# Kernel optimization log

Measured on AMD Instinct MI355X. Metric: run time of the kernel, lower is better.

Reference implementation:

```python
import jax, jax.numpy as jnp
import numpy as np

NUM_USERS = 100000
NUM_ITEMS = 200000
EMB_DIM = 64
NUM_LAYERS = 3
NUM_INTER = 1000000
BATCH = 16384


def setup_inputs() -> dict:
    key = jax.random.key(0)
    k1, k2, k3, k4, k5, k6, k7 = jax.random.split(key, 7)
    # xavier-uniform-ish init for embeddings
    bound_u = float(np.sqrt(6.0 / (NUM_USERS + EMB_DIM)))
    bound_i = float(np.sqrt(6.0 / (NUM_ITEMS + EMB_DIM)))
    user_emb = jax.random.uniform(k1, (NUM_USERS, EMB_DIM), jnp.float32, -bound_u, bound_u)
    item_emb = jax.random.uniform(k2, (NUM_ITEMS, EMB_DIM), jnp.float32, -bound_i, bound_i)
    layer_weights = jax.random.uniform(k3, (NUM_LAYERS + 1,), jnp.float32)
    inter_users = jax.random.randint(k4, (NUM_INTER,), 0, NUM_USERS, jnp.int32)
    inter_items = jax.random.randint(k5, (NUM_INTER,), 0, NUM_ITEMS, jnp.int32)
    user_ids = jax.random.randint(k6, (BATCH,), 0, NUM_USERS, jnp.int32)
    item_ids = jax.random.randint(k7, (BATCH,), 0, NUM_ITEMS, jnp.int32)
    return {
        "user_emb": user_emb,
        "item_emb": item_emb,
        "layer_weights": layer_weights,
        "inter_users": inter_users,
        "inter_items": inter_items,
        "user_ids": user_ids,
        "item_ids": item_ids,
    }


def reference(user_emb, item_emb, layer_weights, inter_users, inter_items, user_ids, item_ids):
    n_users = user_emb.shape[0]
    n_items = item_emb.shape[0]
    n_nodes = n_users + n_items

    # Symmetrized bipartite edge list: (u -> i+n_users) and (i+n_users -> u)
    rows = inter_users
    cols = inter_items + n_users
    src = jnp.concatenate([rows, cols])  # [2E]
    dst = jnp.concatenate([cols, rows])  # [2E]

    # Symmetric degree normalization: D^{-1/2} A D^{-1/2}
    deg = jax.ops.segment_sum(jnp.ones_like(src, dtype=jnp.float32), src,
                              num_segments=n_nodes)
    dinv = jnp.where(deg > 0, jax.lax.rsqrt(jnp.maximum(deg, 1.0)) * (deg > 0), 0.0)
    dinv = jnp.where(deg > 0, deg ** -0.5, 0.0)
    edge_w = dinv[src] * dinv[dst]  # [2E]

    emb = jnp.concatenate([user_emb, item_emb], axis=0)  # [N, D]
    weights = jax.nn.softmax(layer_weights)

    final = weights[0] * emb
    for layer in range(NUM_LAYERS):
        # SpMM: out[src] += w * emb[dst]
        emb = jax.ops.segment_sum(edge_w[:, None] * emb[dst], src,
                                  num_segments=n_nodes)
        final = final + weights[layer + 1] * emb

    u_final = final[:n_users]
    i_final = final[n_users:]

    user_vectors = u_final[user_ids]   # [B, D]
    item_vectors = i_final[item_ids]   # [B, D]
    scores = jnp.sum(user_vectors * item_vectors, axis=1)  # [B]
    return scores
```

## Files before the change

kernel.cpp:

```cpp
#include <hip/hip_runtime.h>
#include <math.h>

#define NUM_USERS 100000
#define NUM_ITEMS 200000
#define N_NODES   300000
#define EMB       64
#define NUM_INTER 1000000
#define N_EDGES   (2 * NUM_INTER)
#define MAX_SLOTS (N_EDGES + 3 * N_NODES + 16)
#define BATCH     16384

#define BSHIFT 9
#define BNODES 512
#define NBKT   ((N_NODES + BNODES - 1) / BNODES)
#define CAP    6144
#define EDGES_PER_BLOCK 4096
#define AB_BLOCKS ((NUM_INTER + EDGES_PER_BLOCK - 1) / EDGES_PER_BLOCK)

#define CONV_BLOCKS ((N_NODES * 8 + 255) / 256)
#define MARK_BLOCKS ((BATCH * 2) / 256)
#define PROP_BLOCKS ((N_NODES * 8 + 255) / 256)

typedef float    vfloat4 __attribute__((ext_vector_type(4)));
typedef int      vint4   __attribute__((ext_vector_type(4)));
typedef _Float16 half8   __attribute__((ext_vector_type(8)));

__global__ __launch_bounds__(256) void bucket_scatter_k(
        const int* __restrict__ iu, const int* __restrict__ ii,
        int* __restrict__ cursor , uint2* __restrict__ pairs) {
    __shared__ int hist[NBKT];
    __shared__ int gbase[NBKT];
    int tid = threadIdx.x;
    for (int b = tid; b < NBKT; b += 256) hist[b] = 0;
    __syncthreads();

    int e0 = blockIdx.x * EDGES_PER_BLOCK;
    int u[16], it[16];
    unsigned pk[32];
    #pragma unroll
    for (int k = 0; k < 16; ++k) {
        int e = e0 + k * 256 + tid;
        bool v = (e < NUM_INTER);
        u[k]  = v ? iu[e] : -1;
        it[k] = v ? (NUM_USERS + ii[e]) : -1;
    }
    #pragma unroll
    for (int k = 0; k < 16; ++k) {
        if (u[k] >= 0) {
            int b0 = u[k] >> BSHIFT;
            int r0 = atomicAdd(&hist[b0], 1);
            pk[2 * k] = ((unsigned)b0 << 13) | (unsigned)r0;
            int b1 = it[k] >> BSHIFT;
            int r1 = atomicAdd(&hist[b1], 1);
            pk[2 * k + 1] = ((unsigned)b1 << 13) | (unsigned)r1;
        }
    }
    __syncthreads();
    for (int b = tid; b < NBKT; b += 256) {
        int c = hist[b];
        if (c) gbase[b] = atomicAdd(&cursor[b * 16], c);
    }
    __syncthreads();
    #pragma unroll
    for (int k = 0; k < 16; ++k) {
        if (u[k] >= 0) {
            unsigned p0 = pk[2 * k];
            int b0 = (int)(p0 >> 13);
            int s0 = gbase[b0] + (int)(p0 & 0x1fffu);
            if (s0 < CAP) pairs[(size_t)b0 * CAP + s0] = make_uint2((unsigned)u[k], (unsigned)it[k]);
            unsigned p1 = pk[2 * k + 1];
            int b1 = (int)(p1 >> 13);
            int s1 = gbase[b1] + (int)(p1 & 0x1fffu);
            if (s1 < CAP) pairs[(size_t)b1 * CAP + s1] = make_uint2((unsigned)it[k], (unsigned)u[k]);
        }
    }
}

__global__ __launch_bounds__(256) void bucket_deg_k(
        const int* __restrict__ cursor, const uint2* __restrict__ pairs,
        int* __restrict__ deg, float* __restrict__ dinv, float* __restrict__ d2,
        float* __restrict__ rcp, int* __restrict__ lofs, int* __restrict__ bkt_padded) {
    __shared__ int cnt[BNODES];
    __shared__ int sc[256];
    int b = blockIdx.x, tid = threadIdx.x;
    cnt[tid] = 0; cnt[tid + 256] = 0;
    __syncthreads();
    int n = cursor[b * 16]; if (n > CAP) n = CAP;
    const uint2* p = pairs + (size_t)b * CAP;
    for (int j = tid; j < n; j += 256)
        atomicAdd(&cnt[p[j].x & (BNODES - 1)], 1);
    __syncthreads();

    int l0 = 2 * tid, l1 = 2 * tid + 1;
    int c0 = cnt[l0], c1 = cnt[l1];
    int p0 = (c0 + 3) & ~3, p1 = (c1 + 3) & ~3;
    int s = p0 + p1;
    sc[tid] = s;
    __syncthreads();
    for (int o = 1; o < 256; o <<= 1) {
        int x = (tid >= o) ? sc[tid - o] : 0;
        __syncthreads();
        sc[tid] += x;
        __syncthreads();
    }
    int excl = sc[tid] - s;
    int g0 = (b << BSHIFT) + l0;
    int g1 = g0 + 1;
    if (g0 < N_NODES) {
        deg[g0] = c0;
        float fd = (float)c0;
        dinv[g0] = (c0 > 0) ? (1.0f / sqrtf(fd)) : 0.0f;
        d2[g0]   = (c0 > 0) ? (1.0f / fd) : 0.0f;
        rcp[g0]  = (c0 > 0) ? sqrtf(fd) : 0.0f;
        lofs[g0] = excl;
    }
    if (g1 < N_NODES) {
        deg[g1] = c1;
        float fd = (float)c1;
        dinv[g1] = (c1 > 0) ? (1.0f / sqrtf(fd)) : 0.0f;
        d2[g1]   = (c1 > 0) ? (1.0f / fd) : 0.0f;
        rcp[g1]  = (c1 > 0) ? sqrtf(fd) : 0.0f;
        lofs[g1] = excl + p0;
    }
    if (tid == 255) bkt_padded[b] = sc[255];
}

__global__ void csr_mid_k(const int* __restrict__ bkt_padded, int* __restrict__ bkt_base,
                          int* __restrict__ row_start,
                          const float* __restrict__ lw, float* __restrict__ w,
                          _Float16* __restrict__ semb, _Float16* __restrict__ z1,
                          _Float16* __restrict__ z2) {
    __shared__ int lds[1024];
    int t = threadIdx.x;
    int v = (t < NBKT) ? bkt_padded[t] : 0;
    lds[t] = v;
    __syncthreads();
    for (int o = 1; o < 1024; o <<= 1) {
        int x = (t >= o) ? lds[t - o] : 0;
        __syncthreads();
        lds[t] += x;
        __syncthreads();
    }
    if (t < NBKT) bkt_base[t] = lds[t] - v;
    if (t == 1023) row_start[N_NODES] = lds[1023];
    if (t < 96) {
        unsigned* p = (t < 32) ? (unsigned*)semb : (t < 64) ? (unsigned*)z1 : (unsigned*)z2;
        p[(size_t)N_NODES * 32 + (t & 31)] = 0u;
    }
    if (t == 0) {
        float a = lw[0], b = lw[1], c = lw[2], d = lw[3];
        float m = fmaxf(fmaxf(a, b), fmaxf(c, d));
        float e0 = expf(a - m), e1 = expf(b - m), e2 = expf(c - m), e3 = expf(d - m);
        float sm = e0 + e1 + e2 + e3;
        w[0] = e0 / sm; w[1] = e1 / sm; w[2] = e2 / sm; w[3] = e3 / sm;
    }
}

__global__ __launch_bounds__(256) void bucket_build_k(
        const int* __restrict__ cursor, const uint2* __restrict__ pairs,
        const int* __restrict__ bkt_base, const int* __restrict__ lofs,
        int* __restrict__ row_start, int* __restrict__ nbr,
        const float* __restrict__ dinv,
        const float* __restrict__ ue, const float* __restrict__ ie,
        _Float16* __restrict__ semb) {
    int bid = blockIdx.x;
    int tid = threadIdx.x;
    if (bid >= NBKT) {
        int t = (bid - NBKT) * 256 + tid;
        int node = t >> 3;
        int q = t & 7;
        if (node >= N_NODES) return;
        const float4* src = (node < NUM_USERS)
            ? (const float4*)ue + (size_t)node * 16
            : (const float4*)ie + (size_t)(node - NUM_USERS) * 16;
        float4 f0 = src[q * 2];
        float4 f1 = src[q * 2 + 1];
        float s = dinv[node];
        half8 h;
        h[0] = (_Float16)(s * f0.x); h[1] = (_Float16)(s * f0.y);
        h[2] = (_Float16)(s * f0.z); h[3] = (_Float16)(s * f0.w);
        h[4] = (_Float16)(s * f1.x); h[5] = (_Float16)(s * f1.y);
        h[6] = (_Float16)(s * f1.z); h[7] = (_Float16)(s * f1.w);
        ((half8*)semb)[(size_t)node * 8 + q] = h;
        return;
    }
    __shared__ int ofs[BNODES];
    __shared__ int cnt2[BNODES];
    int b = bid;
    int base = bkt_base[b];
    {
        int g0 = (b << BSHIFT) + tid;
        int g1 = g0 + 256;
        int o0 = (g0 < N_NODES) ? lofs[g0] : 0;
        int o1 = (g1 < N_NODES) ? lofs[g1] : 0;
        ofs[tid] = o0; ofs[tid + 256] = o1;
        cnt2[tid] = 0; cnt2[tid + 256] = 0;
        if (g0 < N_NODES) row_start[g0] = base + o0;
        if (g1 < N_NODES) row_start[g1] = base + o1;
    }
    __syncthreads();
    int n = cursor[b * 16]; if (n > CAP) n = CAP;
    const uint2* p = pairs + (size_t)b * CAP;
    for (int j = tid; j < n; j += 256) {
        uint2 pr = p[j];
        int l = (int)(pr.x & (BNODES - 1));
        int r = atomicAdd(&cnt2[l], 1);
        nbr[base + ofs[l] + r] = (int)pr.y;
    }
}

__global__ void mark_prop_k(const int* __restrict__ row_start, const int* __restrict__ nbr,
                            const int* __restrict__ deg, const float* __restrict__ d2,
                            const _Float16* __restrict__ semb, _Float16* __restrict__ z1,
                            const int* __restrict__ uid, const int* __restrict__ iid,
                            int* __restrict__ flag) {
    int bid = blockIdx.x;
    if (bid < MARK_BLOCKS) {
        int t = bid * 256 + threadIdx.x;
        int slot = t >> 1;
        int node = (t & 1) ? (NUM_USERS + iid[slot]) : uid[slot];
        flag[node] = 1;
        int beg = row_start[node];
        int lim = beg + deg[node];
        for (int j = beg; j < lim; ++j) flag[nbr[j]] = 1;
        return;
    }
    int t = (bid - MARK_BLOCKS) * 256 + threadIdx.x;
    int node = t >> 3;
    int q = t & 7;
    if (node >= N_NODES) return;
    int beg = row_start[node], end = row_start[node + 1];
    int lim = beg + deg[node];
    const half8* src = (const half8*)semb;
    float a0 = 0.f, a1 = 0.f, a2 = 0.f, a3 = 0.f, a4 = 0.f, a5 = 0.f, a6 = 0.f, a7 = 0.f;
    for (int j = beg; j < end; j += 8) {
        vint4 na = __builtin_nontemporal_load((const vint4*)(nbr + j));
        vint4 nb = __builtin_nontemporal_load((const vint4*)(nbr + j + 4));
        #pragma unroll
        for (int k = 0; k < 8; ++k) {
            int id = (j + k < lim) ? ((k < 4) ? na[k] : nb[k - 4]) : N_NODES;
            half8 h = src[(size_t)id * 8 + q];
            a0 += (float)h[0]; a1 += (float)h[1]; a2 += (float)h[2]; a3 += (float)h[3];
            a4 += (float)h[4]; a5 += (float)h[5]; a6 += (float)h[6]; a7 += (float)h[7];
        }
    }
    float s = d2[node];
    half8 r;
    r[0] = (_Float16)(s * a0); r[1] = (_Float16)(s * a1);
    r[2] = (_Float16)(s * a2); r[3] = (_Float16)(s * a3);
    r[4] = (_Float16)(s * a4); r[5] = (_Float16)(s * a5);
    r[6] = (_Float16)(s * a6); r[7] = (_Float16)(s * a7);
    __builtin_nontemporal_store(r, (half8*)z1 + (size_t)node * 8 + q);
}

__global__ void prop_masked_k(const int* __restrict__ row_start, const int* __restrict__ nbr,
                              const int* __restrict__ deg, const float* __restrict__ d2,
                              const int* __restrict__ flag,
                              const _Float16* __restrict__ in, _Float16* __restrict__ out) {
    int t = blockIdx.x * blockDim.x + threadIdx.x;
    int node = t >> 3;
    int q = t & 7;
    if (node >= N_NODES) return;
    if (!flag[node]) return;
    int beg = row_start[node], end = row_start[node + 1];
    int lim = beg + deg[node];
    const half8* src = (const half8*)in;
    float a0 = 0.f, a1 = 0.f, a2 = 0.f, a3 = 0.f, a4 = 0.f, a5 = 0.f, a6 = 0.f, a7 = 0.f;
    for (int j = beg; j < end; j += 8) {
        vint4 na = __builtin_nontemporal_load((const vint4*)(nbr + j));
        vint4 nb = __builtin_nontemporal_load((const vint4*)(nbr + j + 4));
        #pragma unroll
        for (int k = 0; k < 8; ++k) {
            int id = (j + k < lim) ? ((k < 4) ? na[k] : nb[k - 4]) : N_NODES;
            half8 h = src[(size_t)id * 8 + q];
            a0 += (float)h[0]; a1 += (float)h[1]; a2 += (float)h[2]; a3 += (float)h[3];
            a4 += (float)h[4]; a5 += (float)h[5]; a6 += (float)h[6]; a7 += (float)h[7];
        }
    }
    float s = d2[node];
    half8 r;
    r[0] = (_Float16)(s * a0); r[1] = (_Float16)(s * a1);
    r[2] = (_Float16)(s * a2); r[3] = (_Float16)(s * a3);
    r[4] = (_Float16)(s * a4); r[5] = (_Float16)(s * a5);
    r[6] = (_Float16)(s * a6); r[7] = (_Float16)(s * a7);
    __builtin_nontemporal_store(r, (half8*)out + (size_t)node * 8 + q);
}

__global__ void fused_score_k(const int* __restrict__ row_start, const int* __restrict__ nbr,
                              const int* __restrict__ deg,
                              const float* __restrict__ dinv, const float* __restrict__ rcp,
                              const float* __restrict__ ue, const float* __restrict__ ie,
                              const _Float16* __restrict__ z1, const _Float16* __restrict__ z2,
                              const int* __restrict__ uid, const int* __restrict__ iid,
                              const float* __restrict__ w4, float* __restrict__ out) {
    int t = blockIdx.x * blockDim.x + threadIdx.x;
    int slot = t >> 4;
    if (slot >= BATCH) return;
    int within = t & 15;
    int side = within >> 3;
    int q = within & 7;

    int node;
    const float4* erow;
    if (side == 0) {
        int u = uid[slot];
        node = u;
        erow = (const float4*)ue + (size_t)u * 16;
    } else {
        int ii_ = iid[slot];
        node = NUM_USERS + ii_;
        erow = (const float4*)ie + (size_t)ii_ * 16;
    }

    float w0 = w4[0], w1 = w4[1], w2 = w4[2], w3 = w4[3];
    int beg = row_start[node], end = row_start[node + 1];
    int lim = beg + deg[node];
    const half8* z2v = (const half8*)z2;

    float a0 = 0.f, a1 = 0.f, a2 = 0.f, a3 = 0.f, a4 = 0.f, a5 = 0.f, a6 = 0.f, a7 = 0.f;
    for (int j = beg; j < end; j += 8) {
        vint4 na = __builtin_nontemporal_load((const vint4*)(nbr + j));
        vint4 nb = __builtin_nontemporal_load((const vint4*)(nbr + j + 4));
        #pragma unroll
        for (int k = 0; k < 8; ++k) {
            int id = (j + k < lim) ? ((k < 4) ? na[k] : nb[k - 4]) : N_NODES;
            half8 h = z2v[(size_t)id * 8 + q];
            a0 += (float)h[0]; a1 += (float)h[1]; a2 += (float)h[2]; a3 += (float)h[3];
            a4 += (float)h[4]; a5 += (float)h[5]; a6 += (float)h[6]; a7 += (float)h[7];
        }
    }

    float r  = rcp[node];
    float di = dinv[node];
    float e[8];
    *reinterpret_cast<float4*>(&e[0]) = erow[q * 2];
    *reinterpret_cast<float4*>(&e[4]) = erow[q * 2 + 1];
    half8 h1 = ((const half8*)z1)[(size_t)node * 8 + q];
    half8 h2 = z2v[(size_t)node * 8 + q];
    float acc[8] = {a0, a1, a2, a3, a4, a5, a6, a7};

    float f[8];
    #pragma unroll
    for (int d = 0; d < 8; ++d)
        f[d] = w0 * e[d] + r * (w1 * (float)h1[d] + w2 * (float)h2[d]) + w3 * di * acc[d];

    float p = 0.f;
    #pragma unroll
    for (int d = 0; d < 8; ++d) {
        float o = __shfl_xor(f[d], 8);
        p += f[d] * o;
    }
    p += __shfl_xor(p, 1);
    p += __shfl_xor(p, 2);
    p += __shfl_xor(p, 4);

    if (within == 0) out[slot] = p;
}


extern "C" void kernel_launch(void* const* d_in, const int* in_sizes, int n_in,
                              void* d_out, int out_size, void* d_ws, size_t ws_size,
                              hipStream_t stream) {
    const float* user_emb = (const float*)d_in[0];
    const float* item_emb = (const float*)d_in[1];
    const float* layer_w  = (const float*)d_in[2];
    const int*   inter_u  = (const int*)d_in[3];
    const int*   inter_i  = (const int*)d_in[4];
    const int*   user_ids = (const int*)d_in[5];
    const int*   item_ids = (const int*)d_in[6];
    float* out = (float*)d_out;

    char* base = (char*)d_ws;
    size_t off = 0;
    auto alloc = [&](size_t bytes) -> char* {
        char* p = base + off;
        off = (off + bytes + 255) & ~(size_t)255;
        return p;
    };
    float*    w4        = (float*)    alloc(4 * sizeof(float));
    int*      deg       = (int*)      alloc((size_t)N_NODES * sizeof(int));
    float*    dinv      = (float*)    alloc((size_t)N_NODES * sizeof(float));
    float*    d2        = (float*)    alloc((size_t)N_NODES * sizeof(float));
    float*    rcp       = (float*)    alloc((size_t)N_NODES * sizeof(float));
    int*      lofs      = (int*)      alloc((size_t)N_NODES * sizeof(int));
    int*      row_start = (int*)      alloc(((size_t)N_NODES + 1) * sizeof(int));
    int*      bkt_pad   = (int*)      alloc((size_t)NBKT * sizeof(int));
    int*      bkt_base  = (int*)      alloc((size_t)NBKT * sizeof(int));
    int*      flag      = (int*)      alloc((size_t)N_NODES * sizeof(int));
    int*      cursor    = (int*)      alloc((size_t)NBKT * 16 * sizeof(int));
    uint2*    pairs     = (uint2*)    alloc((size_t)NBKT * CAP * sizeof(uint2));
    int*      csr_nbr   = (int*)      alloc((size_t)MAX_SLOTS * sizeof(int));
    _Float16* semb      = (_Float16*) alloc(((size_t)N_NODES + 1) * EMB * sizeof(_Float16));
    _Float16* zA        = (_Float16*) alloc(((size_t)N_NODES + 1) * EMB * sizeof(_Float16));
    _Float16* zB        = (_Float16*) alloc(((size_t)N_NODES + 1) * EMB * sizeof(_Float16));

    size_t span = (size_t)((char*)cursor - (char*)flag) + (size_t)NBKT * 16 * sizeof(int);
    hipMemsetAsync(flag, 0, span, stream);

    bucket_scatter_k<<<AB_BLOCKS, 256, 0, stream>>>(inter_u, inter_i, cursor, pairs);

    bucket_deg_k<<<NBKT, 256, 0, stream>>>(cursor, pairs, deg, dinv, d2, rcp, lofs, bkt_pad);

    csr_mid_k<<<1, 1024, 0, stream>>>(bkt_pad, bkt_base, row_start, layer_w, w4, semb, zB, zA);

    bucket_build_k<<<NBKT + CONV_BLOCKS, 256, 0, stream>>>(
        cursor, pairs, bkt_base, lofs, row_start, csr_nbr, dinv, user_emb, item_emb, semb);

    mark_prop_k<<<MARK_BLOCKS + PROP_BLOCKS, 256, 0, stream>>>(
        row_start, csr_nbr, deg, d2, semb, zB, user_ids, item_ids, flag);

    prop_masked_k<<<PROP_BLOCKS, 256, 0, stream>>>(
        row_start, csr_nbr, deg, d2, flag, zB, zA);

    fused_score_k<<<(BATCH * 16 + 255) / 256, 256, 0, stream>>>(
        row_start, csr_nbr, deg, dinv, rcp, user_emb, item_emb,
        zB , zA , user_ids, item_ids, w4, out);
}
```

Baseline: 280.4 us.

## Pack bucket pairs into 32-bit codes and move neighbor marking into bucket pass

```diff
diff --git a/kernel.cpp b/kernel.cpp
--- a/kernel.cpp
+++ b/kernel.cpp
@@ -6,8 +6,7 @@
 #define N_NODES   300000
 #define EMB       64
 #define NUM_INTER 1000000
-#define N_EDGES   (2 * NUM_INTER)
-#define MAX_SLOTS (N_EDGES + 3 * N_NODES + 16)
+#define MAX_SLOTS (2 * NUM_INTER + 3 * N_NODES + 16)
 #define BATCH     16384
 
 #define BSHIFT 9
@@ -16,25 +15,36 @@
 #define CAP    6144
 #define EDGES_PER_BLOCK 4096
 #define AB_BLOCKS ((NUM_INTER + EDGES_PER_BLOCK - 1) / EDGES_PER_BLOCK)
+#define QMARK_BLOCKS ((BATCH * 2) / 256)
 
 #define CONV_BLOCKS ((N_NODES * 8 + 255) / 256)
-#define MARK_BLOCKS ((BATCH * 2) / 256)
 #define PROP_BLOCKS ((N_NODES * 8 + 255) / 256)
 
-typedef float    vfloat4 __attribute__((ext_vector_type(4)));
-typedef int      vint4   __attribute__((ext_vector_type(4)));
-typedef _Float16 half8   __attribute__((ext_vector_type(8)));
+typedef int      vint4 __attribute__((ext_vector_type(4)));
+typedef _Float16 half8 __attribute__((ext_vector_type(8)));
+
+#define PMASK 0x7FFFFu
 
 __global__ __launch_bounds__(256) void bucket_scatter_k(
         const int* __restrict__ iu, const int* __restrict__ ii,
-        int* __restrict__ cursor , uint2* __restrict__ pairs) {
+        const int* __restrict__ uid, const int* __restrict__ iid,
+        int* __restrict__ cursor , unsigned* __restrict__ pairs,
+        unsigned char* __restrict__ qflag, int* __restrict__ flag) {
+    int tid = threadIdx.x;
+    if (blockIdx.x < QMARK_BLOCKS) {
+        int t = blockIdx.x * 256 + tid;
+        int node = (t & 1) ? (NUM_USERS + iid[t >> 1]) : uid[t >> 1];
+        qflag[node] = 1;
+        flag[node]  = 1;
+        return;
+    }
     __shared__ int hist[NBKT];
     __shared__ int gbase[NBKT];
-    int tid = threadIdx.x;
+    int bid = blockIdx.x - QMARK_BLOCKS;
     for (int b = tid; b < NBKT; b += 256) hist[b] = 0;
     __syncthreads();
 
-    int e0 = blockIdx.x * EDGES_PER_BLOCK;
+    int e0 = bid * EDGES_PER_BLOCK;
     int u[16], it[16];
     unsigned pk[32];
     #pragma unroll
@@ -67,28 +77,41 @@
             unsigned p0 = pk[2 * k];
             int b0 = (int)(p0 >> 13);
             int s0 = gbase[b0] + (int)(p0 & 0x1fffu);
-            if (s0 < CAP) pairs[(size_t)b0 * CAP + s0] = make_uint2((unsigned)u[k], (unsigned)it[k]);
+            if (s0 < CAP)
+                pairs[(size_t)b0 * CAP + s0] =
+                    ((unsigned)(u[k] & (BNODES - 1)) << 19) | (unsigned)it[k];
             unsigned p1 = pk[2 * k + 1];
             int b1 = (int)(p1 >> 13);
             int s1 = gbase[b1] + (int)(p1 & 0x1fffu);
-            if (s1 < CAP) pairs[(size_t)b1 * CAP + s1] = make_uint2((unsigned)it[k], (unsigned)u[k]);
+            if (s1 < CAP)
+                pairs[(size_t)b1 * CAP + s1] =
+                    ((unsigned)(it[k] & (BNODES - 1)) << 19) | (unsigned)u[k];
         }
     }
 }
 
 __global__ __launch_bounds__(256) void bucket_deg_k(
-        const int* __restrict__ cursor, const uint2* __restrict__ pairs,
+        const int* __restrict__ cursor, const unsigned* __restrict__ pairs,
+        const unsigned char* __restrict__ qflag, int* __restrict__ flag,
         int* __restrict__ deg, float* __restrict__ dinv, float* __restrict__ d2,
         float* __restrict__ rcp, int* __restrict__ lofs, int* __restrict__ bkt_padded) {
     __shared__ int cnt[BNODES];
     __shared__ int sc[256];
+    __shared__ unsigned qf[BNODES / 4];
     int b = blockIdx.x, tid = threadIdx.x;
     cnt[tid] = 0; cnt[tid + 256] = 0;
+    if (tid < BNODES / 4)
+        qf[tid] = ((const unsigned*)(qflag + ((size_t)b << BSHIFT)))[tid];
     __syncthreads();
     int n = cursor[b * 16]; if (n > CAP) n = CAP;
-    const uint2* p = pairs + (size_t)b * CAP;
-    for (int j = tid; j < n; j += 256)
-        atomicAdd(&cnt[p[j].x & (BNODES - 1)], 1);
+    const unsigned* p = pairs + (size_t)b * CAP;
+    const unsigned char* qfb = (const unsigned char*)qf;
+    for (int j = tid; j < n; j += 256) {
+        unsigned code = p[j];
+        int l = (int)(code >> 19);
+        atomicAdd(&cnt[l], 1);
+        if (qfb[l]) flag[code & PMASK] = 1;
+    }
     __syncthreads();
 
     int l0 = 2 * tid, l1 = 2 * tid + 1;
@@ -157,7 +180,7 @@
 }
 
 __global__ __launch_bounds__(256) void bucket_build_k(
-        const int* __restrict__ cursor, const uint2* __restrict__ pairs,
+        const int* __restrict__ cursor, const unsigned* __restrict__ pairs,
         const int* __restrict__ bkt_base, const int* __restrict__ lofs,
         int* __restrict__ row_start, int* __restrict__ nbr,
         const float* __restrict__ dinv,
@@ -200,32 +223,19 @@
     }
     __syncthreads();
     int n = cursor[b * 16]; if (n > CAP) n = CAP;
-    const uint2* p = pairs + (size_t)b * CAP;
+    const unsigned* p = pairs + (size_t)b * CAP;
     for (int j = tid; j < n; j += 256) {
-        uint2 pr = p[j];
-        int l = (int)(pr.x & (BNODES - 1));
+        unsigned code = p[j];
+        int l = (int)(code >> 19);
         int r = atomicAdd(&cnt2[l], 1);
-        nbr[base + ofs[l] + r] = (int)pr.y;
-    }
-}
-
-__global__ void mark_prop_k(const int* __restrict__ row_start, const int* __restrict__ nbr,
-                            const int* __restrict__ deg, const float* __restrict__ d2,
-                            const _Float16* __restrict__ semb, _Float16* __restrict__ z1,
-                            const int* __restrict__ uid, const int* __restrict__ iid,
-                            int* __restrict__ flag) {
-    int bid = blockIdx.x;
-    if (bid < MARK_BLOCKS) {
-        int t = bid * 256 + threadIdx.x;
-        int slot = t >> 1;
-        int node = (t & 1) ? (NUM_USERS + iid[slot]) : uid[slot];
-        flag[node] = 1;
-        int beg = row_start[node];
-        int lim = beg + deg[node];
-        for (int j = beg; j < lim; ++j) flag[nbr[j]] = 1;
-        return;
-    }
-    int t = (bid - MARK_BLOCKS) * 256 + threadIdx.x;
+        nbr[base + ofs[l] + r] = (int)(code & PMASK);
+    }
+}
+
+__global__ void prop_first_k(const int* __restrict__ row_start, const int* __restrict__ nbr,
+                             const int* __restrict__ deg, const float* __restrict__ d2,
+                             const _Float16* __restrict__ semb, _Float16* __restrict__ z1) {
+    int t = blockIdx.x * blockDim.x + threadIdx.x;
     int node = t >> 3;
     int q = t & 7;
     if (node >= N_NODES) return;
@@ -386,9 +396,10 @@
     int*      row_start = (int*)      alloc(((size_t)N_NODES + 1) * sizeof(int));
     int*      bkt_pad   = (int*)      alloc((size_t)NBKT * sizeof(int));
     int*      bkt_base  = (int*)      alloc((size_t)NBKT * sizeof(int));
-    int*      flag      = (int*)      alloc((size_t)N_NODES * sizeof(int));
-    int*      cursor    = (int*)      alloc((size_t)NBKT * 16 * sizeof(int));
-    uint2*    pairs     = (uint2*)    alloc((size_t)NBKT * CAP * sizeof(uint2));
+    int*           flag   = (int*)          alloc((size_t)N_NODES * sizeof(int));
+    unsigned char* qflag  = (unsigned char*)alloc((size_t)N_NODES + 512);
+    int*           cursor = (int*)          alloc((size_t)NBKT * 16 * sizeof(int));
+    unsigned* pairs     = (unsigned*) alloc((size_t)NBKT * CAP * sizeof(unsigned));
     int*      csr_nbr   = (int*)      alloc((size_t)MAX_SLOTS * sizeof(int));
     _Float16* semb      = (_Float16*) alloc(((size_t)N_NODES + 1) * EMB * sizeof(_Float16));
     _Float16* zA        = (_Float16*) alloc(((size_t)N_NODES + 1) * EMB * sizeof(_Float16));
@@ -397,17 +408,19 @@
     size_t span = (size_t)((char*)cursor - (char*)flag) + (size_t)NBKT * 16 * sizeof(int);
     hipMemsetAsync(flag, 0, span, stream);
 
-    bucket_scatter_k<<<AB_BLOCKS, 256, 0, stream>>>(inter_u, inter_i, cursor, pairs);
-
-    bucket_deg_k<<<NBKT, 256, 0, stream>>>(cursor, pairs, deg, dinv, d2, rcp, lofs, bkt_pad);
+    bucket_scatter_k<<<QMARK_BLOCKS + AB_BLOCKS, 256, 0, stream>>>(
+        inter_u, inter_i, user_ids, item_ids, cursor, pairs, qflag, flag);
+
+    bucket_deg_k<<<NBKT, 256, 0, stream>>>(
+        cursor, pairs, qflag, flag, deg, dinv, d2, rcp, lofs, bkt_pad);
 
     csr_mid_k<<<1, 1024, 0, stream>>>(bkt_pad, bkt_base, row_start, layer_w, w4, semb, zB, zA);
 
     bucket_build_k<<<NBKT + CONV_BLOCKS, 256, 0, stream>>>(
         cursor, pairs, bkt_base, lofs, row_start, csr_nbr, dinv, user_emb, item_emb, semb);
 
-    mark_prop_k<<<MARK_BLOCKS + PROP_BLOCKS, 256, 0, stream>>>(
-        row_start, csr_nbr, deg, d2, semb, zB, user_ids, item_ids, flag);
+    prop_first_k<<<PROP_BLOCKS, 256, 0, stream>>>(
+        row_start, csr_nbr, deg, d2, semb, zB);
 
     prop_masked_k<<<PROP_BLOCKS, 256, 0, stream>>>(
         row_start, csr_nbr, deg, d2, flag, zB, zA);
```

New measurement: 271.9 us. 3.0% less time.
